# Optimization experiments

Hardware: AMD Instinct MI355X
Metric: run time of the kernel (lower is better)

Reference implementation:

```python
import jax, jax.numpy as jnp
import numpy as np

# Config (matches init_kwargs)
S = 8            # num_seqs
LQ = 256         # query tokens per sequence (num_tokens = S*LQ = 2048)
SEQ = 2048       # kv seq_len per sequence
BLK = 16         # block size
NBLK_PER_SEQ = SEQ // BLK   # 128 = max_num_blocks_per_seq
NUM_BLKS = S * NBLK_PER_SEQ # 1024
HQ = 32          # num_query_heads
HKV = 8          # num_kv_heads
G = HQ // HKV    # queries per kv head (GQA group)
D = 128          # head_size
WINDOW = 1024    # sliding_window
SCALE = 1.0 / float(np.sqrt(D))


def setup_inputs() -> dict:
    key = jax.random.key(0)
    k1, k2, k3 = jax.random.split(key, 3)
    query = jax.random.normal(k1, (S * LQ, HQ, D), jnp.float32)
    key_cache = jax.random.normal(k2, (NUM_BLKS, BLK, HKV, D), jnp.float32)
    value_cache = jax.random.normal(k3, (NUM_BLKS, BLK, HKV, D), jnp.float32)
    # each sequence owns a contiguous run of blocks; all indices valid (>=0)
    block_tables = jnp.arange(NUM_BLKS, dtype=jnp.int32).reshape(S, NBLK_PER_SEQ)
    seq_lens = jnp.full((S,), SEQ, dtype=jnp.int32)
    query_start_len = (jnp.arange(S + 1, dtype=jnp.int32) * LQ)
    return dict(query=query, key_cache=key_cache, value_cache=value_cache,
                block_tables=block_tables, seq_lens=seq_lens,
                query_start_len=query_start_len)


def reference(query, key_cache, value_cache, block_tables, seq_lens, query_start_len):
    # query: [S*LQ, HQ, D] -> [S, LQ, HKV, G, D]
    q = query.reshape(S, LQ, HKV, G, D)
    # paged KV gather: [S, NBLK_PER_SEQ] -> [S, NBLK_PER_SEQ, BLK, HKV, D] -> [S, SEQ, HKV, D]
    K = key_cache[block_tables].reshape(S, SEQ, HKV, D)
    V = value_cache[block_tables].reshape(S, SEQ, HKV, D)
    # attention scores: [S, HKV, G, LQ, SEQ]
    scores = jnp.einsum('sqhgd,skhd->shgqk', q, K) * SCALE
    # causal + sliding-window mask over absolute positions
    ctx = SEQ - LQ  # context_len (same for all seqs here)
    qpos = ctx + jnp.arange(LQ)          # [LQ] absolute query positions
    kpos = jnp.arange(SEQ)               # [SEQ] absolute key positions
    valid = (kpos[None, :] <= qpos[:, None]) & \
            (qpos[:, None] - kpos[None, :] < WINDOW)   # [LQ, SEQ]
    neg_inf = jnp.asarray(-jnp.inf, scores.dtype)
    scores = jnp.where(valid[None, None, None, :, :], scores, neg_inf)
    probs = jax.nn.softmax(scores, axis=-1)
    # output: [S, LQ, HKV, G, D] -> [S*LQ, HQ, D]
    out = jnp.einsum('shgqk,skhd->sqhgd', probs, V)
    return out.reshape(S * LQ, HQ, D)
```

## Files before the change

### kernel.cpp

```cpp
#include <hip/hip_runtime.h>
#include <stdint.h>

typedef __attribute__((ext_vector_type(8))) short short8;
typedef __attribute__((ext_vector_type(4))) float floatx4;
typedef __attribute__((ext_vector_type(4))) unsigned int uint4v;

#define NSEQ 8
#define BLKSZ 16
#define NBLK_PER_SEQ 128
#define HQN 32
#define HKVN 8
#define GQ 4
#define HD 128
#define WINDOW 1024
#define SCALE 0.08838834764831845f

#define QB 32
#define KVB 32
#define KROW 136
#define VROW 40

#define MFMA16 __builtin_amdgcn_mfma_f32_16x16x32_bf16

static __device__ __forceinline__ unsigned int pack2bf(float lo, float hi) {
    unsigned int a = __builtin_bit_cast(unsigned int, lo) + 0x8000u;
    unsigned int b = __builtin_bit_cast(unsigned int, hi) + 0x8000u;
    return __builtin_amdgcn_perm(b, a, 0x07060302u);
}

__global__ __launch_bounds__(256, 2)
void attn_fwd(const float* __restrict__ qg,
              const float* __restrict__ kg,
              const float* __restrict__ vg,
              const int* __restrict__ bt,
              const int* __restrict__ seqlens,
              const int* __restrict__ qsl,
              float* __restrict__ outg)
{
    __shared__ __align__(16) short Klds[2][KVB][KROW];
    __shared__ __align__(16) short Vt[2][HD][VROW];

    const int tid  = threadIdx.x;
    const int lane = tid & 63;
    const int wave = tid >> 6;
    const int l15  = lane & 15;
    const int lg   = lane >> 4;

    const int b  = blockIdx.x;
    const int h  = b & 7;
    const int qt = (b >> 3) & 7;
    const int s  = b >> 6;
    const int q0 = qt * QB;

    const int qstart = qsl[s];
    const int numq   = qsl[s + 1] - qstart;
    const int slen   = seqlens[s];
    const int ctx    = slen - numq;
    const int hq     = h * GQ + wave;

    short8 qf[2][4];
    #pragma unroll
    for (int nq = 0; nq < 2; ++nq) {
        const float* qrow = qg + ((size_t)(qstart + q0 + nq * 16 + l15) * HQN + hq) * HD;
        #pragma unroll
        for (int kt = 0; kt < 4; ++kt) {
            floatx4 f0 = *(const floatx4*)(qrow + kt * 32 + lg * 8);
            floatx4 f1 = *(const floatx4*)(qrow + kt * 32 + lg * 8 + 4);
            uint4v w;
            w[0] = pack2bf(f0[0] * SCALE, f0[1] * SCALE);
            w[1] = pack2bf(f0[2] * SCALE, f0[3] * SCALE);
            w[2] = pack2bf(f1[0] * SCALE, f1[1] * SCALE);
            w[3] = pack2bf(f1[2] * SCALE, f1[3] * SCALE);
            qf[nq][kt] = __builtin_bit_cast(short8, w);
        }
    }

    floatx4 oacc[2][8];
    #pragma unroll
    for (int nq = 0; nq < 2; ++nq)
        #pragma unroll
        for (int dt = 0; dt < 8; ++dt)
            oacc[nq][dt] = (floatx4){0.f, 0.f, 0.f, 0.f};

    float mrun[2] = {-INFINITY, -INFINITY};
    float lrun[2] = {0.f, 0.f};

    int lo = ctx + q0 - WINDOW + 1; if (lo < 0) lo = 0;
    int hi = ctx + q0 + QB - 1;     if (hi > slen - 1) hi = slen - 1;
    const int t0 = lo / KVB, t1 = hi / KVB;

    const int srow = tid >> 3;
    const int sd0  = (tid & 7) * 16;
    const int k2   = tid & 15;
    const int d0v  = (tid >> 4) * 8;

    floatx4 fk[4], fv[4];

#define LOAD_TILE(kv0_) {                                                            \
        const int kvp = (kv0_) + srow;                                               \
        const int blk = bt[s * NBLK_PER_SEQ + (kvp >> 4)];                           \
        const float* src = kg + (((size_t)blk * BLKSZ + (kvp & 15)) * HKVN + h) * HD + sd0; \
        fk[0] = *(const floatx4*)(src);                                              \
        fk[1] = *(const floatx4*)(src + 4);                                          \
        fk[2] = *(const floatx4*)(src + 8);                                          \
        fk[3] = *(const floatx4*)(src + 12);                                         \
        const int kvv = (kv0_) + 2 * k2;                                             \
        const int blkv = bt[s * NBLK_PER_SEQ + (kvv >> 4)];                          \
        const float* vsrc = vg + (((size_t)blkv * BLKSZ + (kvv & 15)) * HKVN + h) * HD + d0v; \
        fv[0] = *(const floatx4*)(vsrc);                                             \
        fv[1] = *(const floatx4*)(vsrc + 4);                                         \
        fv[2] = *(const floatx4*)(vsrc + (size_t)HKVN * HD);                         \
        fv[3] = *(const floatx4*)(vsrc + (size_t)HKVN * HD + 4);                     \
    }

    LOAD_TILE(t0 * KVB);

    int cur = 0;
    for (int t = t0; t <= t1; ++t) {
        const int kv0 = t * KVB;

        {
            uint4v w;
            w[0] = pack2bf(fk[0][0], fk[0][1]);
            w[1] = pack2bf(fk[0][2], fk[0][3]);
            w[2] = pack2bf(fk[1][0], fk[1][1]);
            w[3] = pack2bf(fk[1][2], fk[1][3]);
            *(uint4v*)&Klds[cur][srow][sd0] = w;
            w[0] = pack2bf(fk[2][0], fk[2][1]);
            w[1] = pack2bf(fk[2][2], fk[2][3]);
            w[2] = pack2bf(fk[3][0], fk[3][1]);
            w[3] = pack2bf(fk[3][2], fk[3][3]);
            *(uint4v*)&Klds[cur][srow][sd0 + 8] = w;
            #pragma unroll
            for (int i = 0; i < 8; ++i) {
                *(unsigned int*)&Vt[cur][d0v + i][2 * k2] =
                    pack2bf(fv[i >> 2][i & 3], fv[2 + (i >> 2)][i & 3]);
            }
        }

        if (t < t1) LOAD_TILE(kv0 + KVB);

        __syncthreads();

        floatx4 sacc[2][2];
        sacc[0][0] = (floatx4){0.f,0.f,0.f,0.f}; sacc[0][1] = (floatx4){0.f,0.f,0.f,0.f};
        sacc[1][0] = (floatx4){0.f,0.f,0.f,0.f}; sacc[1][1] = (floatx4){0.f,0.f,0.f,0.f};
        #pragma unroll
        for (int kt = 0; kt < 4; ++kt) {
            #pragma unroll
            for (int m2 = 0; m2 < 2; ++m2) {
                short8 kf = *(const short8*)&Klds[cur][m2 * 16 + l15][kt * 32 + lg * 8];
                sacc[0][m2] = MFMA16(kf, qf[0][kt], sacc[0][m2], 0, 0, 0);
                sacc[1][m2] = MFMA16(kf, qf[1][kt], sacc[1][m2], 0, 0, 0);
            }
        }

        const bool interior = (kv0 >= ctx + q0 - (WINDOW - QB)) &&
                              (kv0 + KVB - 1 <= ctx + q0);
        short8 pfv[2];
        const int srcA = ((lg & 1) << 5) + l15;
        const int srcB = srcA + 16;
        const bool hiSel = (lg >> 1) != 0;
        #pragma unroll
        for (int nq = 0; nq < 2; ++nq) {
            const int qpos = ctx + q0 + nq * 16 + l15;
            float sv[2][4];
            #pragma unroll
            for (int m2 = 0; m2 < 2; ++m2) {
                #pragma unroll
                for (int r = 0; r < 4; ++r) {
                    float x = sacc[nq][m2][r];
                    if (!interior) {
                        const int kpos = kv0 + m2 * 16 + lg * 4 + r;
                        const bool valid = (kpos <= qpos) && (qpos - kpos < WINDOW);
                        x = valid ? x : -INFINITY;
                    }
                    sv[m2][r] = x;
                }
            }
            float rmax = -INFINITY;
            #pragma unroll
            for (int m2 = 0; m2 < 2; ++m2)
                #pragma unroll
                for (int r = 0; r < 4; ++r)
                    rmax = fmaxf(rmax, sv[m2][r]);
            rmax = fmaxf(rmax, __shfl_xor(rmax, 16));
            rmax = fmaxf(rmax, __shfl_xor(rmax, 32));
            const float mold = mrun[nq];
            const bool defer = __all(rmax <= mold + 8.0f);
            const float mnew = defer ? mold : fmaxf(mold, rmax);
            const float alpha = defer ? 1.0f
                : ((mold == -INFINITY) ? ((mnew == -INFINITY) ? 1.0f : 0.0f)
                                       : __expf(mold - mnew));
            const bool dead = (mnew == -INFINITY);
            float rsum = 0.f;
            #pragma unroll
            for (int m2 = 0; m2 < 2; ++m2)
                #pragma unroll
                for (int r = 0; r < 4; ++r) {
                    float e = dead ? 0.f : __expf(sv[m2][r] - mnew);
                    sv[m2][r] = e;
                    rsum += e;
                }
            rsum += __shfl_xor(rsum, 16);
            rsum += __shfl_xor(rsum, 32);
            lrun[nq] = lrun[nq] * alpha + rsum;
            mrun[nq] = mnew;
            if (!defer) {
                #pragma unroll
                for (int dt = 0; dt < 8; ++dt) {
                    oacc[nq][dt][0] *= alpha; oacc[nq][dt][1] *= alpha;
                    oacc[nq][dt][2] *= alpha; oacc[nq][dt][3] *= alpha;
                }
            }
            unsigned int pk0[2], pk1[2];
            #pragma unroll
            for (int m2 = 0; m2 < 2; ++m2) {
                pk0[m2] = pack2bf(sv[m2][0], sv[m2][1]);
                pk1[m2] = pack2bf(sv[m2][2], sv[m2][3]);
            }
            {
                unsigned int a0 = (unsigned int)__shfl((int)pk0[0], srcA, 64);
                unsigned int a1 = (unsigned int)__shfl((int)pk0[1], srcA, 64);
                unsigned int b0 = (unsigned int)__shfl((int)pk1[0], srcA, 64);
                unsigned int b1 = (unsigned int)__shfl((int)pk1[1], srcA, 64);
                unsigned int c0 = (unsigned int)__shfl((int)pk0[0], srcB, 64);
                unsigned int c1 = (unsigned int)__shfl((int)pk0[1], srcB, 64);
                unsigned int d0 = (unsigned int)__shfl((int)pk1[0], srcB, 64);
                unsigned int d1 = (unsigned int)__shfl((int)pk1[1], srcB, 64);
                uint4v w;
                w[0] = hiSel ? a1 : a0;
                w[1] = hiSel ? b1 : b0;
                w[2] = hiSel ? c1 : c0;
                w[3] = hiSel ? d1 : d0;
                pfv[nq] = __builtin_bit_cast(short8, w);
            }
        }

        #pragma unroll
        for (int dt = 0; dt < 8; ++dt) {
            short8 vfn = *(const short8*)&Vt[cur][dt * 16 + l15][lg * 8];
            oacc[0][dt] = MFMA16(vfn, pfv[0], oacc[0][dt], 0, 0, 0);
            oacc[1][dt] = MFMA16(vfn, pfv[1], oacc[1][dt], 0, 0, 0);
        }

        cur ^= 1;
    }
#undef LOAD_TILE

    #pragma unroll
    for (int nq = 0; nq < 2; ++nq) {
        const float inv = 1.0f / lrun[nq];
        float* orow = outg + ((size_t)(qstart + q0 + nq * 16 + l15) * HQN + hq) * HD + lg * 4;
        #pragma unroll
        for (int dt = 0; dt < 8; ++dt) {
            floatx4 o = oacc[nq][dt];
            o[0] *= inv; o[1] *= inv; o[2] *= inv; o[3] *= inv;
            *(floatx4*)(orow + dt * 16) = o;
        }
    }
}

extern "C" void kernel_launch(void* const* d_in, const int* in_sizes, int n_in,
                              void* d_out, int out_size, void* d_ws, size_t ws_size,
                              hipStream_t stream) {
    const float* q  = (const float*)d_in[0];
    const float* k  = (const float*)d_in[1];
    const float* v  = (const float*)d_in[2];
    const int* btp  = (const int*)d_in[3];
    const int* sl   = (const int*)d_in[4];
    const int* qs   = (const int*)d_in[5];
    float* out      = (float*)d_out;

    attn_fwd<<<dim3(NSEQ * HKVN * 8), 256, 0, stream>>>(q, k, v, btp, sl, qs, out);
}
```

Measured before the change: 92.88 us.

## Switch attention MFMAs from 16x16x32 to 32x32x16 bf16 tiles

Replaces the 16x16x32 bf16 MFMA tiling with 32x32x16 MFMAs for both the QK^T and PV products, so one instruction covers the whole 32-query by 32-key tile per wave. Softmax bookkeeping collapses to a single running max and sum per lane, with fewer cross-lane shuffles, and the P-fragment repacking becomes a xor-32 exchange. The aim is fewer MFMA issues, fewer LDS fragment reads and cheaper softmax reductions. It also changes the LDS access patterns and register layout, which can affect bank conflicts and occupancy.

```diff
diff --git a/kernel.cpp b/kernel.cpp
--- a/kernel.cpp
+++ b/kernel.cpp
@@ -3,6 +3,7 @@
 
 typedef __attribute__((ext_vector_type(8))) short short8;
 typedef __attribute__((ext_vector_type(4))) float floatx4;
+typedef __attribute__((ext_vector_type(16))) float f32x16;
 typedef __attribute__((ext_vector_type(4))) unsigned int uint4v;
 
 #define NSEQ 8
@@ -20,7 +21,7 @@
 #define KROW 136
 #define VROW 40
 
-#define MFMA16 __builtin_amdgcn_mfma_f32_16x16x32_bf16
+#define MFMA32 __builtin_amdgcn_mfma_f32_32x32x16_bf16
 
 static __device__ __forceinline__ unsigned int pack2bf(float lo, float hi) {
     unsigned int a = __builtin_bit_cast(unsigned int, lo) + 0x8000u;
@@ -43,8 +44,8 @@
     const int tid  = threadIdx.x;
     const int lane = tid & 63;
     const int wave = tid >> 6;
-    const int l15  = lane & 15;
-    const int lg   = lane >> 4;
+    const int l31  = lane & 31;
+    const int hi   = lane >> 5;
 
     const int b  = blockIdx.x;
     const int h  = b & 7;
@@ -58,36 +59,34 @@
     const int ctx    = slen - numq;
     const int hq     = h * GQ + wave;
 
-    short8 qf[2][4];
-    #pragma unroll
-    for (int nq = 0; nq < 2; ++nq) {
-        const float* qrow = qg + ((size_t)(qstart + q0 + nq * 16 + l15) * HQN + hq) * HD;
-        #pragma unroll
-        for (int kt = 0; kt < 4; ++kt) {
-            floatx4 f0 = *(const floatx4*)(qrow + kt * 32 + lg * 8);
-            floatx4 f1 = *(const floatx4*)(qrow + kt * 32 + lg * 8 + 4);
+    short8 qf[8];
+    {
+        const float* qrow = qg + ((size_t)(qstart + q0 + l31) * HQN + hq) * HD;
+        #pragma unroll
+        for (int ks = 0; ks < 8; ++ks) {
+            floatx4 f0 = *(const floatx4*)(qrow + ks * 16 + hi * 8);
+            floatx4 f1 = *(const floatx4*)(qrow + ks * 16 + hi * 8 + 4);
             uint4v w;
             w[0] = pack2bf(f0[0] * SCALE, f0[1] * SCALE);
             w[1] = pack2bf(f0[2] * SCALE, f0[3] * SCALE);
             w[2] = pack2bf(f1[0] * SCALE, f1[1] * SCALE);
             w[3] = pack2bf(f1[2] * SCALE, f1[3] * SCALE);
-            qf[nq][kt] = __builtin_bit_cast(short8, w);
-        }
-    }
-
-    floatx4 oacc[2][8];
+            qf[ks] = __builtin_bit_cast(short8, w);
+        }
+    }
+
+    f32x16 oacc[4];
     #pragma unroll
-    for (int nq = 0; nq < 2; ++nq)
-        #pragma unroll
-        for (int dt = 0; dt < 8; ++dt)
-            oacc[nq][dt] = (floatx4){0.f, 0.f, 0.f, 0.f};
-
-    float mrun[2] = {-INFINITY, -INFINITY};
-    float lrun[2] = {0.f, 0.f};
+    for (int dblk = 0; dblk < 4; ++dblk)
+        #pragma unroll
+        for (int i = 0; i < 16; ++i)
+            oacc[dblk][i] = 0.f;
+
+    float mrun = -INFINITY, lrun = 0.f;
 
     int lo = ctx + q0 - WINDOW + 1; if (lo < 0) lo = 0;
-    int hi = ctx + q0 + QB - 1;     if (hi > slen - 1) hi = slen - 1;
-    const int t0 = lo / KVB, t1 = hi / KVB;
+    int hiq = ctx + q0 + QB - 1;    if (hiq > slen - 1) hiq = slen - 1;
+    const int t0 = lo / KVB, t1 = hiq / KVB;
 
     const int srow = tid >> 3;
     const int sd0  = (tid & 7) * 16;
@@ -142,121 +141,109 @@
 
         __syncthreads();
 
-        floatx4 sacc[2][2];
-        sacc[0][0] = (floatx4){0.f,0.f,0.f,0.f}; sacc[0][1] = (floatx4){0.f,0.f,0.f,0.f};
-        sacc[1][0] = (floatx4){0.f,0.f,0.f,0.f}; sacc[1][1] = (floatx4){0.f,0.f,0.f,0.f};
-        #pragma unroll
-        for (int kt = 0; kt < 4; ++kt) {
-            #pragma unroll
-            for (int m2 = 0; m2 < 2; ++m2) {
-                short8 kf = *(const short8*)&Klds[cur][m2 * 16 + l15][kt * 32 + lg * 8];
-                sacc[0][m2] = MFMA16(kf, qf[0][kt], sacc[0][m2], 0, 0, 0);
-                sacc[1][m2] = MFMA16(kf, qf[1][kt], sacc[1][m2], 0, 0, 0);
-            }
+        f32x16 sacc;
+        #pragma unroll
+        for (int i = 0; i < 16; ++i) sacc[i] = 0.f;
+        #pragma unroll
+        for (int ks = 0; ks < 8; ++ks) {
+            short8 kf = *(const short8*)&Klds[cur][l31][ks * 16 + hi * 8];
+            sacc = MFMA32(kf, qf[ks], sacc, 0, 0, 0);
         }
 
         const bool interior = (kv0 >= ctx + q0 - (WINDOW - QB)) &&
                               (kv0 + KVB - 1 <= ctx + q0);
-        short8 pfv[2];
-        const int srcA = ((lg & 1) << 5) + l15;
-        const int srcB = srcA + 16;
-        const bool hiSel = (lg >> 1) != 0;
-        #pragma unroll
-        for (int nq = 0; nq < 2; ++nq) {
-            const int qpos = ctx + q0 + nq * 16 + l15;
-            float sv[2][4];
+        const int qpos = ctx + q0 + l31;
+        float p[16];
+        float rmax = -INFINITY;
+        #pragma unroll
+        for (int r = 0; r < 16; ++r) {
+            float x = sacc[r];
+            if (!interior) {
+                const int kpos = kv0 + (r & 3) + 4 * hi + 8 * (r >> 2);
+                const bool valid = (kpos <= qpos) && (qpos - kpos < WINDOW);
+                x = valid ? x : -INFINITY;
+            }
+            p[r] = x;
+            rmax = fmaxf(rmax, x);
+        }
+        rmax = fmaxf(rmax, __shfl_xor(rmax, 32));
+        const float mold = mrun;
+        const bool defer = __all(rmax <= mold + 8.0f);
+        const float mnew = defer ? mold : fmaxf(mold, rmax);
+        const float alpha = defer ? 1.0f
+            : ((mold == -INFINITY) ? ((mnew == -INFINITY) ? 1.0f : 0.0f)
+                                   : __expf(mold - mnew));
+        const bool dead = (mnew == -INFINITY);
+        float rsum = 0.f;
+        #pragma unroll
+        for (int r = 0; r < 16; ++r) {
+            float e = dead ? 0.f : __expf(p[r] - mnew);
+            p[r] = e;
+            rsum += e;
+        }
+        rsum += __shfl_xor(rsum, 32);
+        lrun = lrun * alpha + rsum;
+        mrun = mnew;
+        if (!defer) {
             #pragma unroll
-            for (int m2 = 0; m2 < 2; ++m2) {
-                #pragma unroll
-                for (int r = 0; r < 4; ++r) {
-                    float x = sacc[nq][m2][r];
-                    if (!interior) {
-                        const int kpos = kv0 + m2 * 16 + lg * 4 + r;
-                        const bool valid = (kpos <= qpos) && (qpos - kpos < WINDOW);
-                        x = valid ? x : -INFINITY;
-                    }
-                    sv[m2][r] = x;
-                }
+            for (int dblk = 0; dblk < 4; ++dblk)
+                oacc[dblk] = oacc[dblk] * alpha;
+        }
+
+        unsigned int c0 = pack2bf(p[0],  p[1]);
+        unsigned int c1 = pack2bf(p[2],  p[3]);
+        unsigned int c2 = pack2bf(p[4],  p[5]);
+        unsigned int c3 = pack2bf(p[6],  p[7]);
+        unsigned int c4 = pack2bf(p[8],  p[9]);
+        unsigned int c5 = pack2bf(p[10], p[11]);
+        unsigned int c6 = pack2bf(p[12], p[13]);
+        unsigned int c7 = pack2bf(p[14], p[15]);
+        unsigned int o0 = (unsigned int)__shfl_xor((int)c0, 32);
+        unsigned int o1 = (unsigned int)__shfl_xor((int)c1, 32);
+        unsigned int o2 = (unsigned int)__shfl_xor((int)c2, 32);
+        unsigned int o3 = (unsigned int)__shfl_xor((int)c3, 32);
+        unsigned int o4 = (unsigned int)__shfl_xor((int)c4, 32);
+        unsigned int o5 = (unsigned int)__shfl_xor((int)c5, 32);
+        unsigned int o6 = (unsigned int)__shfl_xor((int)c6, 32);
+        unsigned int o7 = (unsigned int)__shfl_xor((int)c7, 32);
+        uint4v u0, u1;
+        u0[0] = hi ? o2 : c0;
+        u0[1] = hi ? o3 : c1;
+        u0[2] = hi ? c2 : o0;
+        u0[3] = hi ? c3 : o1;
+        u1[0] = hi ? o6 : c4;
+        u1[1] = hi ? o7 : c5;
+        u1[2] = hi ? c6 : o4;
+        u1[3] = hi ? c7 : o5;
+        short8 pb0 = __builtin_bit_cast(short8, u0);
+        short8 pb1 = __builtin_bit_cast(short8, u1);
+
+        #pragma unroll
+        for (int dblk = 0; dblk < 4; ++dblk) {
+            short8 vf0 = *(const short8*)&Vt[cur][dblk * 32 + l31][hi * 8];
+            short8 vf1 = *(const short8*)&Vt[cur][dblk * 32 + l31][16 + hi * 8];
+            oacc[dblk] = MFMA32(vf0, pb0, oacc[dblk], 0, 0, 0);
+            oacc[dblk] = MFMA32(vf1, pb1, oacc[dblk], 0, 0, 0);
+        }
+
+        cur ^= 1;
+    }
+#undef LOAD_TILE
+
+    {
+        const float inv = 1.0f / lrun;
+        float* orow = outg + ((size_t)(qstart + q0 + l31) * HQN + hq) * HD;
+        #pragma unroll
+        for (int dblk = 0; dblk < 4; ++dblk) {
+            #pragma unroll
+            for (int rq = 0; rq < 4; ++rq) {
+                floatx4 o;
+                o[0] = oacc[dblk][4 * rq + 0] * inv;
+                o[1] = oacc[dblk][4 * rq + 1] * inv;
+                o[2] = oacc[dblk][4 * rq + 2] * inv;
+                o[3] = oacc[dblk][4 * rq + 3] * inv;
+                *(floatx4*)(orow + dblk * 32 + 8 * rq + 4 * hi) = o;
             }
-            float rmax = -INFINITY;
-            #pragma unroll
-            for (int m2 = 0; m2 < 2; ++m2)
-                #pragma unroll
-                for (int r = 0; r < 4; ++r)
-                    rmax = fmaxf(rmax, sv[m2][r]);
-            rmax = fmaxf(rmax, __shfl_xor(rmax, 16));
-            rmax = fmaxf(rmax, __shfl_xor(rmax, 32));
-            const float mold = mrun[nq];
-            const bool defer = __all(rmax <= mold + 8.0f);
-            const float mnew = defer ? mold : fmaxf(mold, rmax);
-            const float alpha = defer ? 1.0f
-                : ((mold == -INFINITY) ? ((mnew == -INFINITY) ? 1.0f : 0.0f)
-                                       : __expf(mold - mnew));
-            const bool dead = (mnew == -INFINITY);
-            float rsum = 0.f;
-            #pragma unroll
-            for (int m2 = 0; m2 < 2; ++m2)
-                #pragma unroll
-                for (int r = 0; r < 4; ++r) {
-                    float e = dead ? 0.f : __expf(sv[m2][r] - mnew);
-                    sv[m2][r] = e;
-                    rsum += e;
-                }
-            rsum += __shfl_xor(rsum, 16);
-            rsum += __shfl_xor(rsum, 32);
-            lrun[nq] = lrun[nq] * alpha + rsum;
-            mrun[nq] = mnew;
-            if (!defer) {
-                #pragma unroll
-                for (int dt = 0; dt < 8; ++dt) {
-                    oacc[nq][dt][0] *= alpha; oacc[nq][dt][1] *= alpha;
-                    oacc[nq][dt][2] *= alpha; oacc[nq][dt][3] *= alpha;
-                }
-            }
-            unsigned int pk0[2], pk1[2];
-            #pragma unroll
-            for (int m2 = 0; m2 < 2; ++m2) {
-                pk0[m2] = pack2bf(sv[m2][0], sv[m2][1]);
-                pk1[m2] = pack2bf(sv[m2][2], sv[m2][3]);
-            }
-            {
-                unsigned int a0 = (unsigned int)__shfl((int)pk0[0], srcA, 64);
-                unsigned int a1 = (unsigned int)__shfl((int)pk0[1], srcA, 64);
-                unsigned int b0 = (unsigned int)__shfl((int)pk1[0], srcA, 64);
-                unsigned int b1 = (unsigned int)__shfl((int)pk1[1], srcA, 64);
-                unsigned int c0 = (unsigned int)__shfl((int)pk0[0], srcB, 64);
-                unsigned int c1 = (unsigned int)__shfl((int)pk0[1], srcB, 64);
-                unsigned int d0 = (unsigned int)__shfl((int)pk1[0], srcB, 64);
-                unsigned int d1 = (unsigned int)__shfl((int)pk1[1], srcB, 64);
-                uint4v w;
-                w[0] = hiSel ? a1 : a0;
-                w[1] = hiSel ? b1 : b0;
-                w[2] = hiSel ? c1 : c0;
-                w[3] = hiSel ? d1 : d0;
-                pfv[nq] = __builtin_bit_cast(short8, w);
-            }
-        }
-
-        #pragma unroll
-        for (int dt = 0; dt < 8; ++dt) {
-            short8 vfn = *(const short8*)&Vt[cur][dt * 16 + l15][lg * 8];
-            oacc[0][dt] = MFMA16(vfn, pfv[0], oacc[0][dt], 0, 0, 0);
-            oacc[1][dt] = MFMA16(vfn, pfv[1], oacc[1][dt], 0, 0, 0);
-        }
-
-        cur ^= 1;
-    }
-#undef LOAD_TILE
-
-    #pragma unroll
-    for (int nq = 0; nq < 2; ++nq) {
-        const float inv = 1.0f / lrun[nq];
-        float* orow = outg + ((size_t)(qstart + q0 + nq * 16 + l15) * HQN + hq) * HD + lg * 4;
-        #pragma unroll
-        for (int dt = 0; dt < 8; ++dt) {
-            floatx4 o = oacc[nq][dt];
-            o[0] *= inv; o[1] *= inv; o[2] *= inv; o[3] *= inv;
-            *(floatx4*)(orow + dt * 16) = o;
         }
     }
 }
```

New measurement: 85.15 us. 8.3% less time.
